# Performance work log

Hardware: AMD Instinct MI355X
Metric: run time of the kernel (lower is better)

## Reference

```python
import jax, jax.numpy as jnp
import numpy as np

B, C_IN, N, C_OUT, K = 16, 64, 2048, 64, 20
BN_EPS = 1e-5
SLOPE = 0.2  # LeakyReLU negative slope


def setup_inputs() -> dict:
    key = jax.random.key(0)
    ks = jax.random.split(key, 6)
    x = jax.random.normal(ks[0], (B, C_IN, N), jnp.float32)
    # Conv2d(2*C_IN, C_OUT, 1, bias=False), kaiming-normal init -> [C_OUT, 2*C_IN]
    W = jax.random.normal(ks[1], (C_OUT, 2 * C_IN), jnp.float32) * np.sqrt(2.0 / (2 * C_IN))
    # BatchNorm2d (eval mode) affine params + running stats
    gamma = jax.random.uniform(ks[2], (C_OUT,), jnp.float32, 0.5, 1.5)
    beta = jax.random.normal(ks[3], (C_OUT,), jnp.float32) * 0.1
    run_mean = jax.random.normal(ks[4], (C_OUT,), jnp.float32) * 0.1
    run_var = jax.random.uniform(ks[5], (C_OUT,), jnp.float32, 0.5, 1.5)
    return {"x": x, "W": W, "gamma": gamma, "beta": beta,
            "run_mean": run_mean, "run_var": run_var}


def _knn(x):
    """x: [B, C, N] -> neighbor indices [B, N, K] (nearest, includes self)."""
    xt = jnp.swapaxes(x, 1, 2)                       # [B, N, C]
    sq = jnp.sum(xt * xt, axis=-1)                   # [B, N]
    # squared euclidean distance; topk of -dist == nearest neighbors
    dist = sq[:, :, None] - 2.0 * jnp.einsum('bnc,bmc->bnm', xt, xt) + sq[:, None, :]
    _, idx = jax.lax.top_k(-dist, K)                 # [B, N, K]
    return idx


def reference(x, W, gamma, beta, run_mean, run_var):
    # --- dynamic graph (knn computed under no_grad in the original) ---
    idx = _knn(jax.lax.stop_gradient(x))             # [B, N, K]
    # --- dual gather: edge_index[1]=neighbors -> x_i, edge_index[0]=centers -> x_j ---
    xt = jnp.swapaxes(x, 1, 2)                       # [B, N, C]
    x_i = jax.vmap(lambda xb, ib: xb[ib])(xt, idx)   # [B, N, K, C] neighbor feats
    x_i = jnp.transpose(x_i, (0, 3, 1, 2))           # [B, C, N, K]
    x_j = x[:, :, :, None]                           # [B, C, N, 1] center feats
    feat = jnp.concatenate([x_i, x_j - x_i], axis=1)  # [B, 2C, N, K]
    # --- 1x1 conv (no bias) ---
    h = jnp.einsum('oc,bcnk->bonk', W, feat)         # [B, C_OUT, N, K]
    # --- BatchNorm2d eval mode, folded affine ---
    inv = gamma / jnp.sqrt(run_var + BN_EPS)
    h = h * inv[None, :, None, None] + (beta - run_mean * inv)[None, :, None, None]
    # --- LeakyReLU(0.2); Dropout(0.0) is identity ---
    h = jnp.where(h > 0, h, SLOPE * h)
    # --- max over neighbors ---
    out = jnp.max(h, axis=-1)                        # [B, C_OUT, N]
    return out, idx
```

## Files before the change

kernel.cpp:

```cpp
#include <hip/hip_runtime.h>
#include <cstdint>
#include <cstddef>

#define B_ 16
#define C_ 64
#define N_ 2048
#define K_ 20
#define CAND 24
#define LQ 12

typedef short bf16x8 __attribute__((ext_vector_type(8)));
typedef float f32x4 __attribute__((ext_vector_type(4)));

__device__ __forceinline__ unsigned umin_(unsigned a, unsigned b) { return a < b ? a : b; }
__device__ __forceinline__ unsigned umax_(unsigned a, unsigned b) { return a > b ? a : b; }
__device__ __forceinline__ unsigned short bfr_(float v) {
    unsigned u = __float_as_uint(v);
    return (unsigned short)((u + 0x7FFFu + ((u >> 16) & 1u)) >> 16);
}

__global__ __launch_bounds__(128) void k_sq(const float* __restrict__ x,
                                            float* __restrict__ sqf,
                                            unsigned short* __restrict__ xh,
                                            float* __restrict__ xrT,
                                            float* __restrict__ Yt,
                                            const float* __restrict__ W) {
    __shared__ float Ag[C_ * 64];
    int tid = threadIdx.x;
    bool doY = (Yt != nullptr);
    if (doY) {
        int o = tid & 63, ch = tid >> 6;
#pragma unroll
        for (int j = 0; j < 32; ++j) {
            int c = ch * 32 + j;
            Ag[c * 64 + o] = W[o * 128 + c] - W[o * 128 + 64 + c];
        }
    }
    int i = blockIdx.x * 128 + tid;
    int b = i >> 11, n = i & (N_ - 1);
    const float* xb = x + (size_t)b * C_ * N_ + n;
    float vr[C_];
#pragma unroll
    for (int c = 0; c < C_; ++c) vr[c] = xb[(size_t)c * N_];
    float p[C_];
#pragma unroll
    for (int c = 0; c < C_; ++c) p[c] = __fmul_rn(vr[c], vr[c]);
    float r[8];
#pragma unroll
    for (int k = 0; k < 8; ++k) r[k] = p[k];
#pragma unroll
    for (int ii = 8; ii < 64; ii += 8) {
#pragma unroll
        for (int k = 0; k < 8; ++k) r[k] = __fadd_rn(r[k], p[ii + k]);
    }
    float s0 = __fadd_rn(__fadd_rn(r[0], r[1]), __fadd_rn(r[2], r[3]));
    float s1 = __fadd_rn(__fadd_rn(r[4], r[5]), __fadd_rn(r[6], r[7]));
    sqf[i] = __fadd_rn(s0, s1);

    unsigned short* xrow = xh + (size_t)i * 64;
#pragma unroll
    for (int cb = 0; cb < 8; ++cb) {
        bf16x8 pk;
#pragma unroll
        for (int e = 0; e < 8; ++e) pk[e] = (short)bfr_(vr[cb * 8 + e]);
        *reinterpret_cast<bf16x8*>(xrow + ((cb ^ (n & 7)) * 8)) = pk;
    }
    if (xrT) {
        float4* dst = reinterpret_cast<float4*>(xrT + (size_t)i * C_);
#pragma unroll
        for (int q = 0; q < 16; ++q)
            dst[q] = make_float4(vr[q*4+0], vr[q*4+1], vr[q*4+2], vr[q*4+3]);
    }
    if (doY) {
        __syncthreads();
        float4 acc[16];
#pragma unroll
        for (int q = 0; q < 16; ++q) acc[q] = make_float4(0.f, 0.f, 0.f, 0.f);
#pragma unroll 4
        for (int c = 0; c < C_; ++c) {
            float xv = vr[c];
            const float4* a4 = reinterpret_cast<const float4*>(&Ag[c * 64]);
#pragma unroll
            for (int q = 0; q < 16; ++q) {
                float4 a = a4[q];
                acc[q].x = fmaf(xv, a.x, acc[q].x);
                acc[q].y = fmaf(xv, a.y, acc[q].y);
                acc[q].z = fmaf(xv, a.z, acc[q].z);
                acc[q].w = fmaf(xv, a.w, acc[q].w);
            }
        }
        float4* yp = reinterpret_cast<float4*>(Yt + (size_t)i * 64);
#pragma unroll
        for (int q = 0; q < 16; ++q) yp[q] = acc[q];
    }
}

__global__ __launch_bounds__(256) void k_y(const float* __restrict__ x,
                                           const float* __restrict__ W,
                                           float* __restrict__ Yt) {
    __shared__ float Al[C_ * 64];
    __shared__ float xl[C_ * 64];
    int tid = threadIdx.x;
    int bid = blockIdx.x;
    int b = bid >> 5;
    int m0 = (bid & 31) * 64;
    {
        int o = tid & 63, cb = tid >> 6;
#pragma unroll
        for (int j = 0; j < 16; ++j) {
            int c = cb * 16 + j;
            Al[c * 64 + o] = W[o * 128 + c] - W[o * 128 + 64 + c];
            xl[c * 64 + o] = x[((size_t)b * C_ + c) * N_ + m0 + o];
        }
    }
    __syncthreads();
    int ml = tid & 63, og = tid >> 6;
    float acc[16];
#pragma unroll
    for (int j = 0; j < 16; ++j) acc[j] = 0.f;
#pragma unroll 4
    for (int c = 0; c < C_; ++c) {
        float xv = xl[c * 64 + ml];
        const float4* a4 = reinterpret_cast<const float4*>(&Al[c * 64 + og * 16]);
#pragma unroll
        for (int q = 0; q < 4; ++q) {
            float4 av = a4[q];
            acc[q*4+0] = fmaf(av.x, xv, acc[q*4+0]);
            acc[q*4+1] = fmaf(av.y, xv, acc[q*4+1]);
            acc[q*4+2] = fmaf(av.z, xv, acc[q*4+2]);
            acc[q*4+3] = fmaf(av.w, xv, acc[q*4+3]);
        }
    }
    float* yp = Yt + ((size_t)b * N_ + m0 + ml) * C_ + og * 16;
#pragma unroll
    for (int q = 0; q < 4; ++q)
        reinterpret_cast<float4*>(yp)[q] =
            make_float4(acc[q*4+0], acc[q*4+1], acc[q*4+2], acc[q*4+3]);
}

__global__ __launch_bounds__(256, 2) void k_dist(const unsigned short* __restrict__ xh,
                                                 const float* __restrict__ sqf,
                                                 unsigned short* __restrict__ candu) {
    __shared__ __align__(16) unsigned short xtl[256 * 64];
    __shared__ float sqm[256];
    int tid = threadIdx.x;
    int w = tid >> 6, lane = tid & 63;
    int bid = blockIdx.x;
    int b = bid >> 5;
    int n0 = (bid & 31) * 64;
    const unsigned short* xhb = xh + (size_t)b * N_ * 64;

    {
#pragma unroll
        for (int i = 0; i < 2; ++i) {
            int ch = tid + 256 * i;
            *reinterpret_cast<uint4*>(&xtl[ch * 8]) =
                *reinterpret_cast<const uint4*>(&xhb[(size_t)n0 * 64 + ch * 8]);
        }
    }
    __syncthreads();
    int rl = w * 16 + (lane & 15);
    int cb0 = (lane >> 4), cb1 = 4 + (lane >> 4);
    bf16x8 afr0 = *reinterpret_cast<const bf16x8*>(&xtl[rl * 64 + ((cb0 ^ (lane & 7)) * 8)]);
    bf16x8 afr1 = *reinterpret_cast<const bf16x8*>(&xtl[rl * 64 + ((cb1 ^ (lane & 7)) * 8)]);
    float rsq[4];
#pragma unroll
    for (int r = 0; r < 4; ++r)
        rsq[r] = sqf[b * N_ + n0 + w * 16 + (lane >> 4) * 4 + r];

    unsigned list[4][LQ];
#pragma unroll
    for (int r = 0; r < 4; ++r)
#pragma unroll
        for (int j = 0; j < LQ; ++j) list[r][j] = 0xFFFFFFFFu;

    for (int t = 0; t < 8; ++t) {
        int m0 = t * 256;
        __syncthreads();
        {
#pragma unroll
            for (int i = 0; i < 8; ++i) {
                int ch = tid + 256 * i;
                *reinterpret_cast<uint4*>(&xtl[ch * 8]) =
                    *reinterpret_cast<const uint4*>(&xhb[(size_t)m0 * 64 + ch * 8]);
            }
            sqm[tid] = sqf[b * N_ + m0 + tid];
        }
        __syncthreads();
        const unsigned short* pB0 = &xtl[(lane & 15) * 64 + ((cb0 ^ (lane & 7)) * 8)];
        const unsigned short* pB1 = &xtl[(lane & 15) * 64 + ((cb1 ^ (lane & 7)) * 8)];
        const float* pS = &sqm[lane & 15];
#pragma unroll
        for (int mb = 0; mb < 16; ++mb) {
            bf16x8 bf0 = *reinterpret_cast<const bf16x8*>(pB0 + mb * 1024);
            bf16x8 bf1 = *reinterpret_cast<const bf16x8*>(pB1 + mb * 1024);
            f32x4 acc = {0.f, 0.f, 0.f, 0.f};
            acc = __builtin_amdgcn_mfma_f32_16x16x32_bf16(afr0, bf0, acc, 0, 0, 0);
            acc = __builtin_amdgcn_mfma_f32_16x16x32_bf16(afr1, bf1, acc, 0, 0, 0);
            float smv = pS[mb * 16];
            unsigned mg = (unsigned)(m0 + mb * 16) | (unsigned)(lane & 15);
#pragma unroll
            for (int r = 0; r < 4; ++r) {
                float rs = rsq[r] + smv;
                float d = fmaf(-2.f, acc[r], rs);
                d = fmaxf(d, 0.f);
                unsigned key = (__float_as_uint(d) & 0xFFFFF800u) | mg;
#pragma unroll
                for (int j = LQ - 1; j > 0; --j)
                    asm("v_med3_u32 %0, %0, %1, %2"
                        : "+v"(list[r][j])
                        : "v"(list[r][j - 1]), "v"(key));
                list[r][0] = umin_(list[r][0], key);
            }
        }
    }

    size_t grow0 = (size_t)b * N_ + n0 + w * 16 + (lane >> 4) * 4;
#pragma unroll 1
    for (int it = 0; it < CAND; ++it) {
        unsigned head[4], wv[4];
#pragma unroll
        for (int j = 0; j < 4; ++j) { head[j] = list[j][0]; wv[j] = head[j]; }
#pragma unroll
        for (int d2 = 1; d2 < 16; d2 <<= 1)
#pragma unroll
            for (int j = 0; j < 4; ++j)
                wv[j] = umin_(wv[j], (unsigned)__shfl_xor((int)wv[j], d2, 16));
#pragma unroll
        for (int j = 0; j < 4; ++j) {
            bool own = (head[j] == wv[j]);
#pragma unroll
            for (int jj = 0; jj < LQ - 1; ++jj)
                list[j][jj] = own ? list[j][jj + 1] : list[j][jj];
            list[j][LQ - 1] = own ? 0xFFFFFFFFu : list[j][LQ - 1];
            if ((lane & 15) == 0)
                candu[(grow0 + j) * CAND + it] = (unsigned short)(wv[j] & 2047u);
        }
    }
}

__global__ __launch_bounds__(256) void k_rescore(const float* __restrict__ x,
                                                 const float* __restrict__ xrT,
                                                 const float* __restrict__ sqf,
                                                 const unsigned short* __restrict__ candu,
                                                 float* __restrict__ idxf) {
    int tid = threadIdx.x;
    int w = tid >> 6, lane = tid & 63;
    size_t grow = (size_t)blockIdx.x * 4 + w;
    int b = (int)(grow >> 11), n = (int)(grow & (N_ - 1));
    float d = 0.f;
    unsigned m = 0xFFFFFFFFu;
    if (xrT) {
        const float* xr = xrT + (size_t)b * N_ * C_;
        const float* xn = xr + (size_t)n * C_;
        if (lane < CAND) {
            m = candu[grow * CAND + lane];
            const float* xm = xr + (size_t)m * C_;
            float a = 0.f;
#pragma unroll 8
            for (int c = 0; c < C_; ++c)
                a = __fadd_rn(a, __fmul_rn(xn[c], xm[c]));
            d = __fadd_rn(__fsub_rn(sqf[b * N_ + n], __fmul_rn(2.0f, a)), sqf[b * N_ + m]);
        }
    } else {
        const float* xb = x + (size_t)b * C_ * N_;
        if (lane < CAND) {
            m = candu[grow * CAND + lane];
            float a = 0.f;
#pragma unroll 8
            for (int c = 0; c < C_; ++c)
                a = __fadd_rn(a, __fmul_rn(xb[(size_t)c * N_ + n], xb[(size_t)c * N_ + m]));
            d = __fadd_rn(__fsub_rn(sqf[b * N_ + n], __fmul_rn(2.0f, a)), sqf[b * N_ + m]);
        }
    }
    int rank = 0;
#pragma unroll 1
    for (int j = 0; j < CAND; ++j) {
        float dj = __shfl(d, j, 64);
        unsigned mj = (unsigned)__shfl((int)m, j, 64);
        if (lane < CAND && (dj < d || (dj == d && mj < m))) ++rank;
    }
    if (lane < CAND && rank < K_)
        idxf[grow * K_ + rank] = (float)m;
}

__global__ __launch_bounds__(256) void k_out(const float* __restrict__ x,
                                             const float* __restrict__ W,
                                             const float* __restrict__ gamma,
                                             const float* __restrict__ beta,
                                             const float* __restrict__ rmean,
                                             const float* __restrict__ rvar,
                                             const float* __restrict__ Yt,
                                             const float* __restrict__ idxf,
                                             float* __restrict__ out) {
    __shared__ float Bl[C_ * 64];
    __shared__ float xl[C_ * 64];
    __shared__ float resl[64 * 65];
    __shared__ float sl[64], tl[64];
    int tid = threadIdx.x;
    int bid = blockIdx.x;
    int b = bid >> 5;
    int n0 = (bid & 31) * 64;
    {
        int o = tid & 63, cb = tid >> 6;
#pragma unroll
        for (int j = 0; j < 16; ++j) {
            int c = cb * 16 + j;
            Bl[c * 64 + o] = W[o * 128 + 64 + c];
            xl[c * 64 + o] = x[((size_t)b * C_ + c) * N_ + n0 + o];
        }
        if (tid < 64) {
            float s = gamma[tid] / sqrtf(rvar[tid] + 1e-5f);
            sl[tid] = s;
            tl[tid] = beta[tid] - rmean[tid] * s;
        }
    }
    __syncthreads();
    int w = tid >> 6, o = tid & 63;
    for (int i = 0; i < 16; ++i) {
        int nl = w * 16 + i;
        int n = n0 + nl;
        float u = 0.f;
#pragma unroll 8
        for (int c = 0; c < C_; ++c)
            u = fmaf(Bl[c * 64 + o], xl[c * 64 + nl], u);
        const float* ip = idxf + ((size_t)b * N_ + n) * K_;
        float v = -3.4e38f;
#pragma unroll
        for (int k = 0; k < K_; ++k) {
            int mi = (int)ip[k];
            v = fmaxf(v, Yt[((size_t)b * N_ + mi) * C_ + o]);
        }
        float h = u + v;
        float val = sl[o] * h + tl[o];
        val = val > 0.f ? val : 0.2f * val;
        resl[o * 65 + nl] = val;
    }
    __syncthreads();
    {
        int nl = tid & 63, ob = tid >> 6;
#pragma unroll
        for (int j = 0; j < 16; ++j) {
            int o2 = ob * 16 + j;
            out[((size_t)b * C_ + o2) * N_ + n0 + nl] = resl[o2 * 65 + nl];
        }
    }
}

extern "C" void kernel_launch(void* const* d_in, const int* in_sizes, int n_in,
                              void* d_out, int out_size, void* d_ws, size_t ws_size,
                              hipStream_t stream) {
    const float* x     = (const float*)d_in[0];
    const float* W     = (const float*)d_in[1];
    const float* gamma = (const float*)d_in[2];
    const float* beta  = (const float*)d_in[3];
    const float* rmean = (const float*)d_in[4];
    const float* rvar  = (const float*)d_in[5];

    float* out  = (float*)d_out;
    float* idxf = out + (size_t)B_ * C_ * N_;

    char* ws = (char*)d_ws;
    float* sqf            = (float*)ws;
    unsigned short* candu = (unsigned short*)(ws + 131072);
    unsigned short* xh    = (unsigned short*)(ws + 131072 + 1572864);
    size_t off_xrT        = 131072 + 1572864 + 4194304;
    size_t need_xrT       = off_xrT + 8388608;
    size_t need_fused     = need_xrT + 8388608;
    float* xrT            = (ws_size >= need_xrT) ? (float*)(ws + off_xrT) : nullptr;
    bool fused            = (ws_size >= need_fused);
    float* Yt             = fused ? (float*)(ws + need_xrT) : (float*)(ws + 131072);

    k_sq     <<<B_ * N_ / 128, 128, 0, stream>>>(x, sqf, xh, xrT, fused ? Yt : nullptr, W);
    k_dist   <<<B_ * 32, 256, 0, stream>>>(xh, sqf, candu);
    k_rescore<<<B_ * N_ / 4, 256, 0, stream>>>(x, xrT, sqf, candu, idxf);
    if (!fused)
        k_y  <<<B_ * (N_ / 64), 256, 0, stream>>>(x, W, Yt);
    k_out    <<<B_ * (N_ / 64), 256, 0, stream>>>(x, W, gamma, beta, rmean, rvar, Yt, idxf, out);
}
```

Baseline: 176.4 us.

## Fuse candidate rescoring into k_dist and vectorize k_out neighbor max

Candidate lists are kept in shared memory and rescored in fp32 inside k_dist when the transposed fp32 copy exists. This removes the separate k_rescore launch and the candidate round trip through global memory. k_out is restructured so each thread handles one point and four output channels at a time, using float4 loads of Yt rows and of the weights, with the neighbor indices preloaded into registers. The cost is extra shared memory in k_dist, which may reduce occupancy, and a serial rescoring tail inside each distance block.

Result: no change. 174.6 us (-1.0%).

```diff
diff --git a/kernel.cpp b/kernel.cpp
--- a/kernel.cpp
+++ b/kernel.cpp
@@ -140,9 +140,13 @@
 
 __global__ __launch_bounds__(256, 2) void k_dist(const unsigned short* __restrict__ xh,
                                                  const float* __restrict__ sqf,
+                                                 const float* __restrict__ xrT,
+                                                 float* __restrict__ idxf,
                                                  unsigned short* __restrict__ candu) {
     __shared__ __align__(16) unsigned short xtl[256 * 64];
     __shared__ float sqm[256];
+    __shared__ unsigned short cl[64][CAND];
+    __shared__ float dl2[64][CAND];
     int tid = threadIdx.x;
     int w = tid >> 6, lane = tid & 63;
     int bid = blockIdx.x;
@@ -215,7 +219,9 @@
         }
     }
 
-    size_t grow0 = (size_t)b * N_ + n0 + w * 16 + (lane >> 4) * 4;
+    int rowl0 = w * 16 + (lane >> 4) * 4;
+    size_t grow0 = (size_t)b * N_ + n0 + rowl0;
+    bool fusedR = (xrT != nullptr);
 #pragma unroll 1
     for (int it = 0; it < CAND; ++it) {
         unsigned head[4], wv[4];
@@ -233,14 +239,68 @@
             for (int jj = 0; jj < LQ - 1; ++jj)
                 list[j][jj] = own ? list[j][jj + 1] : list[j][jj];
             list[j][LQ - 1] = own ? 0xFFFFFFFFu : list[j][LQ - 1];
-            if ((lane & 15) == 0)
-                candu[(grow0 + j) * CAND + it] = (unsigned short)(wv[j] & 2047u);
-        }
+            if ((lane & 15) == 0) {
+                if (fusedR) cl[rowl0 + j][it] = (unsigned short)(wv[j] & 2047u);
+                else        candu[(grow0 + j) * CAND + it] = (unsigned short)(wv[j] & 2047u);
+            }
+        }
+    }
+
+    if (!fusedR) return;
+
+    __syncthreads();
+    float* xnl = reinterpret_cast<float*>(xtl);
+    const float* xr = xrT + (size_t)b * N_ * C_;
+    {
+        const float4* src = reinterpret_cast<const float4*>(xr + (size_t)n0 * C_);
+#pragma unroll
+        for (int q = 0; q < 4; ++q) {
+            int idx = tid + q * 256;
+            reinterpret_cast<float4*>(xnl)[idx] = src[idx];
+        }
+    }
+    __syncthreads();
+    int bN = b * N_;
+#pragma unroll 1
+    for (int t2 = 0; t2 < 6; ++t2) {
+        int task = tid + t2 * 256;
+        int row = task / 24, ci = task - row * 24;
+        int m = cl[row][ci];
+        const float* xn = xnl + row * 64;
+        const float* xm = xr + (size_t)m * C_;
+        float a = 0.f;
+#pragma unroll
+        for (int cq = 0; cq < 16; ++cq) {
+            float4 n4 = *reinterpret_cast<const float4*>(xn + cq * 4);
+            float4 m4 = *reinterpret_cast<const float4*>(xm + cq * 4);
+            a = __fadd_rn(a, __fmul_rn(n4.x, m4.x));
+            a = __fadd_rn(a, __fmul_rn(n4.y, m4.y));
+            a = __fadd_rn(a, __fmul_rn(n4.z, m4.z));
+            a = __fadd_rn(a, __fmul_rn(n4.w, m4.w));
+        }
+        dl2[row][ci] = __fadd_rn(__fsub_rn(sqf[bN + n0 + row], __fmul_rn(2.0f, a)),
+                                 sqf[bN + m]);
+    }
+    __syncthreads();
+#pragma unroll 1
+    for (int t2 = 0; t2 < 6; ++t2) {
+        int task = tid + t2 * 256;
+        int row = task / 24, ci = task - row * 24;
+        int m = cl[row][ci];
+        float di = dl2[row][ci];
+        int rank = 0;
+#pragma unroll
+        for (int j = 0; j < CAND; ++j) {
+            float dj = dl2[row][j];
+            int mj = cl[row][j];
+            rank += (dj < di || (dj == di && mj < m)) ? 1 : 0;
+        }
+        if (rank < K_)
+            idxf[((size_t)bN + n0 + row) * K_ + rank] = (float)m;
     }
 }
 
 __global__ __launch_bounds__(256) void k_rescore(const float* __restrict__ x,
-                                                 const float* __restrict__ xrT,
                                                  const float* __restrict__ sqf,
                                                  const unsigned short* __restrict__ candu,
                                                  float* __restrict__ idxf) {
@@ -248,30 +308,16 @@
     int w = tid >> 6, lane = tid & 63;
     size_t grow = (size_t)blockIdx.x * 4 + w;
     int b = (int)(grow >> 11), n = (int)(grow & (N_ - 1));
+    const float* xb = x + (size_t)b * C_ * N_;
     float d = 0.f;
     unsigned m = 0xFFFFFFFFu;
-    if (xrT) {
-        const float* xr = xrT + (size_t)b * N_ * C_;
-        const float* xn = xr + (size_t)n * C_;
-        if (lane < CAND) {
-            m = candu[grow * CAND + lane];
-            const float* xm = xr + (size_t)m * C_;
-            float a = 0.f;
+    if (lane < CAND) {
+        m = candu[grow * CAND + lane];
+        float a = 0.f;
 #pragma unroll 8
-            for (int c = 0; c < C_; ++c)
-                a = __fadd_rn(a, __fmul_rn(xn[c], xm[c]));
-            d = __fadd_rn(__fsub_rn(sqf[b * N_ + n], __fmul_rn(2.0f, a)), sqf[b * N_ + m]);
-        }
-    } else {
-        const float* xb = x + (size_t)b * C_ * N_;
-        if (lane < CAND) {
-            m = candu[grow * CAND + lane];
-            float a = 0.f;
-#pragma unroll 8
-            for (int c = 0; c < C_; ++c)
-                a = __fadd_rn(a, __fmul_rn(xb[(size_t)c * N_ + n], xb[(size_t)c * N_ + m]));
-            d = __fadd_rn(__fsub_rn(sqf[b * N_ + n], __fmul_rn(2.0f, a)), sqf[b * N_ + m]);
-        }
+        for (int c = 0; c < C_; ++c)
+            a = __fadd_rn(a, __fmul_rn(xb[(size_t)c * N_ + n], xb[(size_t)c * N_ + m]));
+        d = __fadd_rn(__fsub_rn(sqf[b * N_ + n], __fmul_rn(2.0f, a)), sqf[b * N_ + m]);
     }
     int rank = 0;
 #pragma unroll 1
@@ -316,33 +362,56 @@
         }
     }
     __syncthreads();
-    int w = tid >> 6, o = tid & 63;
-    for (int i = 0; i < 16; ++i) {
-        int nl = w * 16 + i;
-        int n = n0 + nl;
-        float u = 0.f;
+    int nl = tid & 63, wv2 = tid >> 6;
+    const float* ip = idxf + ((size_t)b * N_ + n0 + nl) * K_;
+    int mi[K_];
+#pragma unroll
+    for (int k = 0; k < K_; ++k) mi[k] = (int)ip[k];
+    const float* Ytb = Yt + (size_t)b * N_ * C_;
+#pragma unroll
+    for (int t = 0; t < 4; ++t) {
+        int oq = wv2 * 4 + t;
+        float ax = 0.f, ay = 0.f, az = 0.f, aw = 0.f;
 #pragma unroll 8
-        for (int c = 0; c < C_; ++c)
-            u = fmaf(Bl[c * 64 + o], xl[c * 64 + nl], u);
-        const float* ip = idxf + ((size_t)b * N_ + n) * K_;
-        float v = -3.4e38f;
+        for (int c = 0; c < C_; ++c) {
+            float xv = xl[c * 64 + nl];
+            float4 bl4 = *reinterpret_cast<const float4*>(&Bl[c * 64 + oq * 4]);
+            ax = fmaf(bl4.x, xv, ax);
+            ay = fmaf(bl4.y, xv, ay);
+            az = fmaf(bl4.z, xv, az);
+            aw = fmaf(bl4.w, xv, aw);
+        }
+        float vx = -3.4e38f, vy = -3.4e38f, vz = -3.4e38f, vw = -3.4e38f;
 #pragma unroll
         for (int k = 0; k < K_; ++k) {
-            int mi = (int)ip[k];
-            v = fmaxf(v, Yt[((size_t)b * N_ + mi) * C_ + o]);
-        }
-        float h = u + v;
-        float val = sl[o] * h + tl[o];
-        val = val > 0.f ? val : 0.2f * val;
-        resl[o * 65 + nl] = val;
+            float4 y4 = *reinterpret_cast<const float4*>(&Ytb[(size_t)mi[k] * C_ + oq * 4]);
+            vx = fmaxf(vx, y4.x);
+            vy = fmaxf(vy, y4.y);
+            vz = fmaxf(vz, y4.z);
+            vw = fmaxf(vw, y4.w);
+        }
+        float h0 = ax + vx, h1 = ay + vy, h2 = az + vz, h3 = aw + vw;
+        int o0 = oq * 4;
+        float v0 = sl[o0 + 0] * h0 + tl[o0 + 0];
+        float v1 = sl[o0 + 1] * h1 + tl[o0 + 1];
+        float v2 = sl[o0 + 2] * h2 + tl[o0 + 2];
+        float v3 = sl[o0 + 3] * h3 + tl[o0 + 3];
+        v0 = v0 > 0.f ? v0 : 0.2f * v0;
+        v1 = v1 > 0.f ? v1 : 0.2f * v1;
+        v2 = v2 > 0.f ? v2 : 0.2f * v2;
+        v3 = v3 > 0.f ? v3 : 0.2f * v3;
+        resl[(o0 + 0) * 65 + nl] = v0;
+        resl[(o0 + 1) * 65 + nl] = v1;
+        resl[(o0 + 2) * 65 + nl] = v2;
+        resl[(o0 + 3) * 65 + nl] = v3;
     }
     __syncthreads();
     {
-        int nl = tid & 63, ob = tid >> 6;
+        int nl2 = tid & 63, ob = tid >> 6;
 #pragma unroll
         for (int j = 0; j < 16; ++j) {
             int o2 = ob * 16 + j;
-            out[((size_t)b * C_ + o2) * N_ + n0 + nl] = resl[o2 * 65 + nl];
+            out[((size_t)b * C_ + o2) * N_ + n0 + nl2] = resl[o2 * 65 + nl2];
         }
     }
 }
@@ -372,8 +441,9 @@
     float* Yt             = fused ? (float*)(ws + need_xrT) : (float*)(ws + 131072);
 
     k_sq     <<<B_ * N_ / 128, 128, 0, stream>>>(x, sqf, xh, xrT, fused ? Yt : nullptr, W);
-    k_dist   <<<B_ * 32, 256, 0, stream>>>(xh, sqf, candu);
-    k_rescore<<<B_ * N_ / 4, 256, 0, stream>>>(x, xrT, sqf, candu, idxf);
+    k_dist   <<<B_ * 32, 256, 0, stream>>>(xh, sqf, xrT, idxf, candu);
+    if (!xrT)
+        k_rescore<<<B_ * N_ / 4, 256, 0, stream>>>(x, sqf, candu, idxf);
     if (!fused)
         k_y  <<<B_ * (N_ / 64), 256, 0, stream>>>(x, W, Yt);
     k_out    <<<B_ * (N_ / 64), 256, 0, stream>>>(x, W, gamma, beta, rmean, rvar, Yt, idxf, out);
```
